# Kernel optimization log

Hardware: AMD Instinct MI355X
Metric: run time of the kernel (lower is better)

The kernel has to match this reference:

```python
import jax, jax.numpy as jnp
import numpy as np

N_NODES = 100000
N_EDGES = 1600000
NODE_DIM = 32
EDGE_DIM = 16
OUT_DIM = 32


def setup_inputs() -> dict:
    key = jax.random.key(0)
    ks = jax.random.split(key, 8)
    D = NODE_DIM + EDGE_DIM  # 48
    return {
        "y": jax.random.normal(ks[0], (N_NODES, NODE_DIM), dtype=jnp.float32),
        "ex": jax.random.normal(ks[1], (N_EDGES, EDGE_DIM), dtype=jnp.float32),
        "W1": jax.random.normal(ks[2], (D, D), dtype=jnp.float32) / np.sqrt(D),
        "b1": jax.random.normal(ks[3], (D,), dtype=jnp.float32) * 0.01,
        "W2": jax.random.normal(ks[4], (OUT_DIM, D), dtype=jnp.float32) / np.sqrt(D),
        "b2": jax.random.normal(ks[5], (OUT_DIM,), dtype=jnp.float32) * 0.01,
        "src": jax.random.randint(ks[6], (N_EDGES,), 0, N_NODES, dtype=jnp.int32),
        "dst": jax.random.randint(ks[7], (N_EDGES,), 0, N_NODES, dtype=jnp.int32),
    }


def reference(y, ex, W1, b1, W2, b2, src, dst):
    n_nodes = y.shape[0]
    # per-edge message: ReLU(Linear(concat(y[src], e_x)))  -> [E, node_dim+edge_dim]
    feat = jnp.concatenate([y[src], ex], axis=1)
    m = jax.nn.relu(feat @ W1.T + b1)
    # mean scatter-reduce onto destination nodes (0 for isolated nodes, DGL semantics)
    s = jax.ops.segment_sum(m, dst, num_segments=n_nodes)
    cnt = jax.ops.segment_sum(jnp.ones((m.shape[0],), m.dtype), dst, num_segments=n_nodes)
    z = jnp.where(cnt[:, None] > 0, s / jnp.maximum(cnt, 1.0)[:, None], 0.0)
    # node update: ReLU(Linear(z)) -> [N, out_dim]
    h = jax.nn.relu(z @ W2.T + b2)
    return h
```

## Files before the change

### kernel.cpp

```cpp
#include <hip/hip_runtime.h>

#define NODE_DIM 32
#define EDGE_DIM 16
#define DD 48
#define OUT_DIM 32
#define MAXDEG 64
#define STAGED 32
#define NXCD 8
#define NPW 16

typedef _Float16 f16x8 __attribute__((ext_vector_type(8)));
typedef float f32x4 __attribute__((ext_vector_type(4)));

__global__ __launch_bounds__(256)
void prep_kernel(const float* __restrict__ y, _Float16* __restrict__ yh, int CBy,
                 const float* __restrict__ ex, _Float16* __restrict__ exh,
                 int N, int E) {
    int b = blockIdx.x;
    if (b < CBy) {
        size_t i = ((size_t)b * 256 + threadIdx.x) * 8;
        if (i < (size_t)N * NODE_DIM) {
            const float4* s0 = reinterpret_cast<const float4*>(y + i);
            const float4 a = s0[0], c = s0[1];
            f16x8 h = {(_Float16)a.x, (_Float16)a.y, (_Float16)a.z, (_Float16)a.w,
                       (_Float16)c.x, (_Float16)c.y, (_Float16)c.z, (_Float16)c.w};
            *reinterpret_cast<f16x8*>(yh + i) = h;
        }
        return;
    }
    b -= CBy;
    size_t i = ((size_t)b * 256 + threadIdx.x) * 8;
    if (i < (size_t)E * EDGE_DIM) {
        const float4* s0 = reinterpret_cast<const float4*>(ex + i);
        const float4 a = s0[0], c = s0[1];
        f16x8 h = {(_Float16)a.x, (_Float16)a.y, (_Float16)a.z, (_Float16)a.w,
                   (_Float16)c.x, (_Float16)c.y, (_Float16)c.z, (_Float16)c.w};
        *reinterpret_cast<f16x8*>(exh + i) = h;
    }
}

__global__ __launch_bounds__(256)
void scatter_kernel(const int* __restrict__ dst, const int* __restrict__ src,
                    int* __restrict__ cursor, int2* __restrict__ meta,
                    int E, int NP) {
    const int xcd = blockIdx.x & (NXCD - 1);
    const int c   = blockIdx.x >> 3;
    const int base = c * 2048 + threadIdx.x * 8;
    if (base >= E) return;

    int dv[8], sv[8];
    if (base + 8 <= E) {
        *reinterpret_cast<int4*>(dv)     = *reinterpret_cast<const int4*>(dst + base);
        *reinterpret_cast<int4*>(dv + 4) = *reinterpret_cast<const int4*>(dst + base + 4);
        *reinterpret_cast<int4*>(sv)     = *reinterpret_cast<const int4*>(src + base);
        *reinterpret_cast<int4*>(sv + 4) = *reinterpret_cast<const int4*>(src + base + 4);
    } else {
#pragma unroll
        for (int i = 0; i < 8; ++i) {
            dv[i] = (base + i < E) ? dst[base + i] : -1;
            sv[i] = (base + i < E) ? src[base + i] : 0;
        }
    }
#pragma unroll
    for (int i = 0; i < 8; ++i) {
        const int d = dv[i];
        if (d >= 0 && (d & (NXCD - 1)) == xcd && base + i < E) {
            int pos = atomicAdd(&cursor[xcd * NP + (d >> 3)], 1);
            if (pos < MAXDEG)
                meta[(size_t)d * MAXDEG + pos] = make_int2(base + i, sv[i]);
        }
    }
}

__global__ __launch_bounds__(256)
void fused_kernel(const _Float16* __restrict__ yh, const _Float16* __restrict__ exh,
                  const float* __restrict__ W1, const float* __restrict__ b1,
                  const float* __restrict__ W2, const float* __restrict__ b2,
                  const int* __restrict__ cursor, const int2* __restrict__ meta,
                  float* __restrict__ out, int N, int NP) {
    __shared__ int2 mlds[4][NPW][STAGED];
    __shared__ _Float16 zl[4][NPW][64];

    const int wave = threadIdx.x >> 6;
    const int lane = threadIdx.x & 63;
    const int col = lane & 15;
    const int kg  = lane >> 4;

    f16x8 Blo[3], Bhi[3];
#pragma unroll
    for (int t = 0; t < 3; ++t) {
        const float* wr = W1 + (size_t)(t * 16 + col) * DD;
#pragma unroll
        for (int j = 0; j < 8; ++j) {
            Blo[t][j] = (_Float16)wr[kg * 8 + j];
            Bhi[t][j] = (_Float16)0.f;
        }
        if (kg < 2) {
#pragma unroll
            for (int j = 0; j < 8; ++j)
                Bhi[t][j] = (_Float16)wr[NODE_DIM + kg * 8 + j];
        }
        if (kg == 3) Bhi[t][7] = (_Float16)b1[t * 16 + col];
    }

    const int nb0 = (blockIdx.x * 4 + wave) * NPW;

    int dgv = 0;
    if (lane < NPW) {
        const int n = nb0 + lane;
        if (n < N) dgv = cursor[(n & (NXCD - 1)) * NP + (n >> 3)];
    }

#pragma unroll
    for (int ni = 0; ni < NPW; ++ni) {
        const int cnt_i = min(__shfl(dgv, ni), STAGED);
        const int n = nb0 + ni;
        if (lane < STAGED)
            mlds[wave][ni][lane] = (lane < cnt_i && n < N)
                                       ? meta[(size_t)n * MAXDEG + lane]
                                       : make_int2(0, 0);
    }
    __builtin_amdgcn_wave_barrier();

    for (int ni = 0; ni < NPW; ++ni) {
        const int n = nb0 + ni;
        const int dg = __shfl(dgv, ni);
        const int cnt = min(dg, MAXDEG);

        float pacc0 = 0.f, pacc1 = 0.f, pacc2 = 0.f;
        const int ngroups = (cnt + 15) >> 4;

        for (int g = 0; g < ngroups; ++g) {
            const int row = g * 16 + col;
            const bool valid = row < cnt;
            const int2 md = (row < STAGED)
                                ? mlds[wave][ni][row]
                                : (valid ? meta[(size_t)n * MAXDEG + row]
                                         : make_int2(0, 0));
            const int eid = md.x, sv = md.y;

            f16x8 alo = *reinterpret_cast<const f16x8*>(
                yh + (size_t)sv * NODE_DIM + kg * 8);

            f16x8 ahi;
            if (kg < 2) {
                ahi = *reinterpret_cast<const f16x8*>(
                    exh + (size_t)eid * EDGE_DIM + kg * 8);
            } else {
#pragma unroll
                for (int j = 0; j < 8; ++j) ahi[j] = (_Float16)0.f;
                if (kg == 3) ahi[7] = (_Float16)1.f;
            }

            if (!valid) {
#pragma unroll
                for (int j = 0; j < 8; ++j) { alo[j] = (_Float16)0.f; ahi[j] = (_Float16)0.f; }
            }

#pragma unroll
            for (int t = 0; t < 3; ++t) {
                f32x4 c = {0.f, 0.f, 0.f, 0.f};
                c = __builtin_amdgcn_mfma_f32_16x16x32_f16(alo, Blo[t], c, 0, 0, 0);
                c = __builtin_amdgcn_mfma_f32_16x16x32_f16(ahi, Bhi[t], c, 0, 0, 0);
#pragma unroll
                for (int r = 0; r < 4; ++r) {
                    const float v = fmaxf(c[r], 0.f);
                    if (t == 0) pacc0 += v;
                    else if (t == 1) pacc1 += v;
                    else pacc2 += v;
                }
            }
        }

        pacc0 += __shfl_xor(pacc0, 16); pacc0 += __shfl_xor(pacc0, 32);
        pacc1 += __shfl_xor(pacc1, 16); pacc1 += __shfl_xor(pacc1, 32);
        pacc2 += __shfl_xor(pacc2, 16); pacc2 += __shfl_xor(pacc2, 32);

        if (n < N) {
            const float inv = (dg > 0) ? 1.f / (float)dg : 0.f;
            if (lane < 16) {
                zl[wave][ni][lane]      = (_Float16)(pacc0 * inv);
                zl[wave][ni][lane + 16] = (_Float16)(pacc1 * inv);
                zl[wave][ni][lane + 32] = (_Float16)(pacc2 * inv);
            }
            if (lane < 8) {
                const unsigned int v = (lane == 0) ? 0x00003C00u : 0u;
                *reinterpret_cast<unsigned int*>(&zl[wave][ni][48 + lane * 2]) = v;
            }
        } else if (lane < 32) {
            *reinterpret_cast<unsigned int*>(&zl[wave][ni][lane * 2]) = 0u;
        }
    }

    f16x8 Wf[2][2];
#pragma unroll
    for (int t = 0; t < 2; ++t) {
#pragma unroll
        for (int c = 0; c < 2; ++c) {
            f16x8 v;
#pragma unroll
            for (int j = 0; j < 8; ++j) {
                const int k = c * 32 + kg * 8 + j;
                float w = 0.f;
                if (k < DD)       w = W2[(size_t)(t * 16 + col) * DD + k];
                else if (k == DD) w = b2[t * 16 + col];
                v[j] = (_Float16)w;
            }
            Wf[t][c] = v;
        }
    }

    __builtin_amdgcn_wave_barrier();
    const _Float16* zr = &zl[wave][col][0];
    const f16x8 A0 = *reinterpret_cast<const f16x8*>(zr + kg * 8);
    const f16x8 A1 = *reinterpret_cast<const f16x8*>(zr + 32 + kg * 8);

#pragma unroll
    for (int t = 0; t < 2; ++t) {
        f32x4 h = {0.f, 0.f, 0.f, 0.f};
        h = __builtin_amdgcn_mfma_f32_16x16x32_f16(A0, Wf[t][0], h, 0, 0, 0);
        h = __builtin_amdgcn_mfma_f32_16x16x32_f16(A1, Wf[t][1], h, 0, 0, 0);
#pragma unroll
        for (int r = 0; r < 4; ++r) {
            const int node = nb0 + kg * 4 + r;
            if (node < N)
                out[(size_t)node * OUT_DIM + t * 16 + col] = fmaxf(h[r], 0.f);
        }
    }
}

extern "C" void kernel_launch(void* const* d_in, const int* in_sizes, int n_in,
                              void* d_out, int out_size, void* d_ws, size_t ws_size,
                              hipStream_t stream) {
    const float* y  = (const float*)d_in[0];
    const float* ex = (const float*)d_in[1];
    const float* W1 = (const float*)d_in[2];
    const float* b1 = (const float*)d_in[3];
    const float* W2 = (const float*)d_in[4];
    const float* b2 = (const float*)d_in[5];
    const int* src  = (const int*)d_in[6];
    const int* dst  = (const int*)d_in[7];

    const int N = in_sizes[0] / NODE_DIM;
    const int E = in_sizes[6];
    const int NP = (N + NXCD - 1) / NXCD;
    const int NC = ((NXCD * NP + 3) / 4) * 4;

    int* cursor = (int*)d_ws;
    size_t off  = ((size_t)NC * sizeof(int) + 255) & ~(size_t)255;
    int2* meta  = (int2*)((char*)d_ws + off);
    _Float16* yh = (_Float16*)((char*)meta + (size_t)N * MAXDEG * sizeof(int2));
    _Float16* exh = (_Float16*)((char*)yh + (size_t)N * NODE_DIM * sizeof(_Float16));

    const int CBy = (N * NODE_DIM / 8 + 255) / 256;
    const int CBe = (E * EDGE_DIM / 8 + 255) / 256;

    hipMemsetAsync(cursor, 0, (size_t)NC * sizeof(int), stream);

    prep_kernel<<<CBy + CBe, 256, 0, stream>>>(y, yh, CBy, ex, exh, N, E);

    const int K = (E + 2047) / 2048;
    scatter_kernel<<<K * NXCD, 256, 0, stream>>>(dst, src, cursor, meta, E, NP);

    const int NB = (N + NPW * 4 - 1) / (NPW * 4);
    fused_kernel<<<NB, 256, 0, stream>>>(yh, exh, W1, b1, W2, b2,
                                         cursor, meta, (float*)d_out, N, NP);
}
```

Measured before the change: 197.6 us.

## Merge fp16 conversion and CSR scatter into one interleaved launch; halve nodes per wave

```diff
diff --git a/kernel.cpp b/kernel.cpp
--- a/kernel.cpp
+++ b/kernel.cpp
@@ -7,68 +7,73 @@
 #define MAXDEG 64
 #define STAGED 32
 #define NXCD 8
-#define NPW 16
+#define NPW 8
 
 typedef _Float16 f16x8 __attribute__((ext_vector_type(8)));
 typedef float f32x4 __attribute__((ext_vector_type(4)));
 
 __global__ __launch_bounds__(256)
-void prep_kernel(const float* __restrict__ y, _Float16* __restrict__ yh, int CBy,
-                 const float* __restrict__ ex, _Float16* __restrict__ exh,
-                 int N, int E) {
-    int b = blockIdx.x;
-    if (b < CBy) {
-        size_t i = ((size_t)b * 256 + threadIdx.x) * 8;
+void prep_scatter_kernel(const int* __restrict__ dst, const int* __restrict__ src,
+                         int* __restrict__ cursor, int2* __restrict__ meta,
+                         int E, int NP, int K, int G,
+                         const float* __restrict__ y, _Float16* __restrict__ yh,
+                         int CBy, const float* __restrict__ ex,
+                         _Float16* __restrict__ exh, int N) {
+    const int b  = blockIdx.x;
+    const int g  = b >> 3;
+    const int r8 = b & 7;
+    const long long gk = (long long)g * K;
+    const int s0 = (int)(gk / G);
+    const int s1 = (int)((gk + K) / G);
+
+    if (s1 > s0) {
+        const int base = s0 * 2048 + threadIdx.x * 8;
+        if (base >= E) return;
+        int dv[8], sv[8];
+        if (base + 8 <= E) {
+            *reinterpret_cast<int4*>(dv)     = *reinterpret_cast<const int4*>(dst + base);
+            *reinterpret_cast<int4*>(dv + 4) = *reinterpret_cast<const int4*>(dst + base + 4);
+            *reinterpret_cast<int4*>(sv)     = *reinterpret_cast<const int4*>(src + base);
+            *reinterpret_cast<int4*>(sv + 4) = *reinterpret_cast<const int4*>(src + base + 4);
+        } else {
+#pragma unroll
+            for (int i = 0; i < 8; ++i) {
+                dv[i] = (base + i < E) ? dst[base + i] : -1;
+                sv[i] = (base + i < E) ? src[base + i] : 0;
+            }
+        }
+#pragma unroll
+        for (int i = 0; i < 8; ++i) {
+            const int d = dv[i];
+            if (d >= 0 && (d & (NXCD - 1)) == r8 && base + i < E) {
+                int pos = atomicAdd(&cursor[r8 * NP + (d >> 3)], 1);
+                if (pos < MAXDEG)
+                    meta[(size_t)d * MAXDEG + pos] = make_int2(base + i, sv[i]);
+            }
+        }
+        return;
+    }
+
+    int cb = (g - s0) * 8 + r8;
+    if (cb < CBy) {
+        size_t i = ((size_t)cb * 256 + threadIdx.x) * 8;
         if (i < (size_t)N * NODE_DIM) {
-            const float4* s0 = reinterpret_cast<const float4*>(y + i);
-            const float4 a = s0[0], c = s0[1];
+            const float4* p = reinterpret_cast<const float4*>(y + i);
+            const float4 a = p[0], c = p[1];
             f16x8 h = {(_Float16)a.x, (_Float16)a.y, (_Float16)a.z, (_Float16)a.w,
                        (_Float16)c.x, (_Float16)c.y, (_Float16)c.z, (_Float16)c.w};
             *reinterpret_cast<f16x8*>(yh + i) = h;
         }
         return;
     }
-    b -= CBy;
-    size_t i = ((size_t)b * 256 + threadIdx.x) * 8;
+    cb -= CBy;
+    size_t i = ((size_t)cb * 256 + threadIdx.x) * 8;
     if (i < (size_t)E * EDGE_DIM) {
-        const float4* s0 = reinterpret_cast<const float4*>(ex + i);
-        const float4 a = s0[0], c = s0[1];
+        const float4* p = reinterpret_cast<const float4*>(ex + i);
+        const float4 a = p[0], c = p[1];
         f16x8 h = {(_Float16)a.x, (_Float16)a.y, (_Float16)a.z, (_Float16)a.w,
                    (_Float16)c.x, (_Float16)c.y, (_Float16)c.z, (_Float16)c.w};
         *reinterpret_cast<f16x8*>(exh + i) = h;
-    }
-}
-
-__global__ __launch_bounds__(256)
-void scatter_kernel(const int* __restrict__ dst, const int* __restrict__ src,
-                    int* __restrict__ cursor, int2* __restrict__ meta,
-                    int E, int NP) {
-    const int xcd = blockIdx.x & (NXCD - 1);
-    const int c   = blockIdx.x >> 3;
-    const int base = c * 2048 + threadIdx.x * 8;
-    if (base >= E) return;
-
-    int dv[8], sv[8];
-    if (base + 8 <= E) {
-        *reinterpret_cast<int4*>(dv)     = *reinterpret_cast<const int4*>(dst + base);
-        *reinterpret_cast<int4*>(dv + 4) = *reinterpret_cast<const int4*>(dst + base + 4);
-        *reinterpret_cast<int4*>(sv)     = *reinterpret_cast<const int4*>(src + base);
-        *reinterpret_cast<int4*>(sv + 4) = *reinterpret_cast<const int4*>(src + base + 4);
-    } else {
-#pragma unroll
-        for (int i = 0; i < 8; ++i) {
-            dv[i] = (base + i < E) ? dst[base + i] : -1;
-            sv[i] = (base + i < E) ? src[base + i] : 0;
-        }
-    }
-#pragma unroll
-    for (int i = 0; i < 8; ++i) {
-        const int d = dv[i];
-        if (d >= 0 && (d & (NXCD - 1)) == xcd && base + i < E) {
-            int pos = atomicAdd(&cursor[xcd * NP + (d >> 3)], 1);
-            if (pos < MAXDEG)
-                meta[(size_t)d * MAXDEG + pos] = make_int2(base + i, sv[i]);
-        }
     }
 }
 
@@ -211,7 +216,7 @@
     }
 
     __builtin_amdgcn_wave_barrier();
-    const _Float16* zr = &zl[wave][col][0];
+    const _Float16* zr = &zl[wave][col & (NPW - 1)][0];
     const f16x8 A0 = *reinterpret_cast<const f16x8*>(zr + kg * 8);
     const f16x8 A1 = *reinterpret_cast<const f16x8*>(zr + 32 + kg * 8);
 
@@ -222,8 +227,9 @@
         h = __builtin_amdgcn_mfma_f32_16x16x32_f16(A1, Wf[t][1], h, 0, 0, 0);
 #pragma unroll
         for (int r = 0; r < 4; ++r) {
-            const int node = nb0 + kg * 4 + r;
-            if (node < N)
+            const int mrow = kg * 4 + r;
+            const int node = nb0 + mrow;
+            if (mrow < NPW && node < N)
                 out[(size_t)node * OUT_DIM + t * 16 + col] = fmaxf(h[r], 0.f);
         }
     }
@@ -254,13 +260,15 @@
 
     const int CBy = (N * NODE_DIM / 8 + 255) / 256;
     const int CBe = (E * EDGE_DIM / 8 + 255) / 256;
+    const int K   = (E + 2047) / 2048;
+    const int CG  = (CBy + CBe + 7) / 8;
+    const int G   = K + CG;
 
     hipMemsetAsync(cursor, 0, (size_t)NC * sizeof(int), stream);
 
-    prep_kernel<<<CBy + CBe, 256, 0, stream>>>(y, yh, CBy, ex, exh, N, E);
-
-    const int K = (E + 2047) / 2048;
-    scatter_kernel<<<K * NXCD, 256, 0, stream>>>(dst, src, cursor, meta, E, NP);
+    prep_scatter_kernel<<<G * 8, 256, 0, stream>>>(dst, src, cursor, meta,
+                                                   E, NP, K, G,
+                                                   y, yh, CBy, ex, exh, N);
 
     const int NB = (N + NPW * 4 - 1) / (NPW * 4);
     fused_kernel<<<NB, 256, 0, stream>>>(yh, exh, W1, b1, W2, b2,
```

Result: faster. 173.7 us (-12.1%).
